# Performance work log

Measured on AMD Instinct MI355X. Metric: run time of the kernel, lower is better.

## Reference

```python
import jax, jax.numpy as jnp
import numpy as np

B, DIM_IN, DIM_OUT, K, A, P = 4, 128, 128, 13, 12, 1024


def _icosahedron_indices():
    """Rebuild the trace/inv index buffers of BasicS2Conv from icosahedron geometry.
    Returns kidx3, aidx3 of shape (K, A, A) = (13, 12, 12) such that the doubly-gathered
    weight is W_full[d,c,k,a,r] = W[d,c, kidx3[k,a,r], aidx3[k,a,r]]."""
    phi = (1.0 + 5.0 ** 0.5) / 2.0
    vs = []
    for s1 in (1.0, -1.0):
        for s2 in (1.0, -1.0):
            vs += [[0.0, s1, s2 * phi], [s1, s2 * phi, 0.0], [s2 * phi, 0.0, s1]]
    vs = np.asarray(vs, dtype=np.float64)
    vs /= np.linalg.norm(vs, axis=1, keepdims=True)
    dots = vs @ vs.T
    order = np.argsort(-dots, axis=1)
    v_adjs = order[:, 1:6]      # 5 adjacent vertices (dot = +1/sqrt5)
    v_level2s = order[:, 6:11]  # 5 second-ring vertices (dot = -1/sqrt5)
    v_opps = order[:, 11]       # antipodal vertex

    def frame(i):
        z = vs[i]
        a = vs[v_adjs[i, 0]]
        x = a - (a @ z) * z
        x /= np.linalg.norm(x)
        y = np.cross(z, x)
        return np.stack([x, y, z], axis=1)

    F0 = frame(0)
    Rs = np.stack([frame(i) @ F0.T for i in range(A)])  # 12 vertex-aligned rotations
    sim = np.einsum('rij,aj,bi->rab', Rs, vs, vs)       # <R_r v_a, v_b>
    trace_idx_rot = np.argmax(sim, axis=1)              # (12, 12) permutations

    inv_idxs = np.empty(K, dtype=np.int64)
    inv_idxs[0] = 0
    inv_idxs[v_adjs[0]] = 1
    inv_idxs[v_level2s[0]] = 2
    inv_idxs[v_opps[0]] = 3
    inv_idxs[12] = 4

    trace_idxv_rot = np.concatenate([trace_idx_rot, np.full((A, 1), 12, dtype=np.int64)], axis=1)  # (12, 13)
    kidx = inv_idxs[trace_idxv_rot].T  # (13, 12): kidx[k, r]
    aidx = trace_idx_rot.T             # (12, 12): aidx[a, r]
    kidx3 = np.broadcast_to(kidx[:, None, :], (K, A, A)).copy()
    aidx3 = np.broadcast_to(aidx[None, :, :], (K, A, A)).copy()
    return kidx3.astype(np.int32), aidx3.astype(np.int32)


def setup_inputs() -> dict:
    key = jax.random.key(0)
    kx, kw = jax.random.split(key)
    x = jax.random.normal(kx, (B, DIM_IN, K, P, A), dtype=jnp.float32)
    # xavier-normal-ish scale for W (dim_out, dim_in, 5, anchor)
    fan = DIM_IN * 5 * A + DIM_OUT * 5 * A
    std = (2.0 ** 0.5) * (2.0 / fan) ** 0.5
    W = jax.random.normal(kw, (DIM_OUT, DIM_IN, 5, A), dtype=jnp.float32) * std
    kidx3, aidx3 = _icosahedron_indices()
    return {"x": x, "W": W, "kidx": jnp.asarray(kidx3), "aidx": jnp.asarray(aidx3)}


def reference(x, W, kidx, aidx):
    # Double gather: W (d, c, 5, A) -> W_full (d, c, K, A, A_rot)
    # W_full[d, c, k, a, r] = W[d, c, kidx[k, a, r], aidx[k, a, r]]
    W_full = W[:, :, kidx, aidx]
    # contraction over kernel point k, input channel c, anchor a
    return jnp.einsum('dckar,bckpa->bdpr', W_full, x)
```

## Files before the change

### kernel.cpp

```cpp
#include <hip/hip_runtime.h>
#include <hip/hip_bf16.h>

typedef __bf16 bf16x8 __attribute__((ext_vector_type(8)));
typedef __bf16 bf16x4 __attribute__((ext_vector_type(4)));
typedef float f32x4 __attribute__((ext_vector_type(4)));
typedef float f32x3 __attribute__((ext_vector_type(3)));
typedef unsigned int u32x3 __attribute__((ext_vector_type(3)));
typedef unsigned short u16;
typedef unsigned int u32;

#define B_   4
#define C_   128
#define K_   13
#define A_   12
#define P_   1024
#define D_   128
#define R_   12
#define NB   1024

#define AS1 __attribute__((address_space(1)))
#define AS3 __attribute__((address_space(3)))

__device__ __forceinline__ u16 f2bf(float f) {
    u32 u = __builtin_bit_cast(u32, f);
    u32 r = (u + 0x7FFFu + ((u >> 16) & 1u)) >> 16;
    return (u16)r;
}
__device__ __forceinline__ float bf2f(u16 v) {
    u32 u = (u32)v << 16;
    return __builtin_bit_cast(float, u);
}
__device__ __forceinline__ u32 pack2(float lo, float hi) {
    return (u32)f2bf(lo) | ((u32)f2bf(hi) << 16);
}

__device__ __forceinline__ void barrier_() {
    asm volatile("" ::: "memory");
    __builtin_amdgcn_s_barrier();
    asm volatile("" ::: "memory");
}
__device__ __forceinline__ void lgkm0_() {
    asm volatile("s_waitcnt lgkmcnt(0)" ::: "memory");
    __builtin_amdgcn_sched_barrier(0);
}
#define VMW(n) asm volatile("s_waitcnt vmcnt(" #n ")" ::: "memory")

__global__ __launch_bounds__(512) void poolk_b(const float* __restrict__ xb_,
                                               const int* __restrict__ kidx3,
                                               u16* __restrict__ pool) {
    const int c  = blockIdx.x;
    const int pp = blockIdx.y;
    const int t  = threadIdx.x;
    const int ah = t & 1, aoff = ah * 6;

    u32 m1[12];
#pragma unroll
    for (int k = 0; k < 12; ++k) {
        u32 m = 0;
#pragma unroll
        for (int r = 0; r < 12; ++r)
            m |= (kidx3[k * 144 + r] == 1 ? 1u : 0u) << r;
        m1[k] = m;
    }

    const float* xb = xb_ + (size_t)c * (K_ * (size_t)P_ * A_);
    const size_t cslab   = (size_t)c * NB * 12;
    const size_t jstride = (size_t)C_ * NB * 12;

    int p = pp * 256 + (t >> 1);
    size_t obase = cslab + (size_t)p * 12 + aoff;
    float T[6] = {0.f, 0.f, 0.f, 0.f, 0.f, 0.f};
    float N[12][6];
#pragma unroll
    for (int r = 0; r < 12; ++r)
#pragma unroll
        for (int j = 0; j < 6; ++j) N[r][j] = 0.f;

#pragma unroll
    for (int k = 0; k < 13; ++k) {
        const float* s = xb + (size_t)k * (P_ * A_) + p * 12 + aoff;
        f32x3 v0 = *(const f32x3*)s;
        f32x3 v1 = *(const f32x3*)(s + 3);
        float v[6] = {v0.x, v0.y, v0.z, v1.x, v1.y, v1.z};
        u32x3 o;
        o.x = pack2(v[0], v[1]); o.y = pack2(v[2], v[3]); o.z = pack2(v[4], v[5]);
        *(u32x3*)(pool + (size_t)k * jstride + obase) = o;
        if (k < 12) {
#pragma unroll
            for (int j = 0; j < 6; ++j) T[j] += v[j];
            u32 m = m1[k];
#pragma unroll
            for (int r = 0; r < 12; ++r) {
                if (m & (1u << r)) {
#pragma unroll
                    for (int j = 0; j < 6; ++j) N[r][j] += v[j];
                }
            }
        }
    }
    {
        u32x3 o;
        o.x = pack2(T[0], T[1]); o.y = pack2(T[2], T[3]); o.z = pack2(T[4], T[5]);
        *(u32x3*)(pool + (size_t)13 * jstride + obase) = o;
    }
#pragma unroll
    for (int r = 0; r < 12; ++r) {
        u32x3 o;
        o.x = pack2(N[r][0], N[r][1]); o.y = pack2(N[r][2], N[r][3]); o.z = pack2(N[r][4], N[r][5]);
        *(u32x3*)(pool + (size_t)(14 + r) * jstride + obase) = o;
    }
}

__global__ __launch_bounds__(256) void abuild(const float* __restrict__ W,
                                              const int* __restrict__ aidx3,
                                              u16* __restrict__ Ab) {
    int gidx = blockIdx.x * 256 + threadIdx.x;
    int r   = gidx / (128 * 960);
    int rem = gidx - r * (128 * 960);
    int d   = rem / 960;
    int p8  = rem - d * 960;
    int phys = p8 * 8;
    int tile = phys / 96;
    int w96  = phys - tile * 96;
    int ks   = w96 >> 5;
    int chp  = (w96 >> 3) & 3;
    int ch   = chp ^ ((d >> 1) & 3);
    int qbase = tile * 96 + ks * 32 + ch * 8;
    u16 o[8];
#pragma unroll
    for (int e = 0; e < 8; ++e) {
        int q  = qbase + e;
        int g  = q / 1536;
        int qq = q - g * 1536;
        int c  = qq / 12;
        int a  = qq - c * 12;
        int aa = aidx3[a * 12 + r];
        const float* wb = W + ((size_t)(d * C_ + c) * 5) * 12 + aa;
        float val;
        if (g == 2)      val = wb[2 * 12];
        else if (g == 4) val = wb[4 * 12];
        else             val = wb[g * 12] - wb[2 * 12];
        o[e] = f2bf(val);
    }
    uint4 v;
    v.x = (u32)o[0] | ((u32)o[1] << 16);
    v.y = (u32)o[2] | ((u32)o[3] << 16);
    v.z = (u32)o[4] | ((u32)o[5] << 16);
    v.w = (u32)o[6] | ((u32)o[7] << 16);
    *(uint4*)(Ab + (((size_t)(r * 80 + tile) * 128 + d) * 96 + w96)) = v;
}

__global__ __launch_bounds__(512) void gemmSb(const u16* __restrict__ Ab,
                                              const u16* __restrict__ pool,
                                              const int* __restrict__ kidx3,
                                              u16* __restrict__ Ctb) {
    __shared__ __align__(16) u16 sA[2][128 * 96];
    __shared__ __align__(16) u16 sB[2][8 * 256 * 12];

    int bx = blockIdx.x;
    int r  = bx % 12;
    int nt = (bx / 12) & 3;
    int sp = bx / 48;
    int n0 = nt * 256;

    int k0r = 0, k3r = 0;
    for (int k = 0; k < 13; ++k) {
        int kv = kidx3[k * 144 + r];
        if (kv == 0) k0r = k;
        if (kv == 3) k3r = k;
    }
    int j = (sp == 0) ? k0r : (sp == 1) ? (14 + r) : (sp == 2) ? 13
          : (sp == 3) ? k3r : 12;

    int lane = threadIdx.x & 63;
    int w    = threadIdx.x >> 6;
    int wm   = w >> 2, wn = w & 3;
    int lq   = lane & 15;

    auto stageA = [&](int buf, int u) {
        const char* src = (const char*)(Ab + (size_t)(r * 80 + sp * 16 + u) * (128 * 96))
                        + w * 3072 + lane * 16;
#pragma unroll
        for (int i = 0; i < 3; ++i)
            __builtin_amdgcn_global_load_lds(
                (const AS1 void*)(src + i * 1024),
                (AS3 void*)&sA[buf][w * 1536 + i * 512],
                16, 0, 0);
    };
    auto stageB = [&](int buf, int u) {
        const char* src = (const char*)(pool + ((size_t)(j * C_ + u * 8 + w) * NB + n0) * 12)
                        + lane * 16;
#pragma unroll
        for (int i = 0; i < 6; ++i)
            __builtin_amdgcn_global_load_lds(
                (const AS1 void*)(src + i * 1024),
                (AS3 void*)&sB[buf][w * 3072 + i * 512],
                16, 0, 0);
    };
    auto ldA = [&](int buf, int m, int ks) -> bf16x8 {
        int ch = (lane >> 4) ^ ((m >> 1) & 3);
        return *(const bf16x8*)&sA[buf][m * 96 + ks * 32 + ch * 8];
    };
    auto ldB = [&](int buf, int n, int ks) -> bf16x8 {
        int q0 = ks * 32 + (lane >> 4) * 8;
        int c1 = q0 / 12, a1 = q0 - c1 * 12;
        int q2 = q0 + 4;
        int c2 = q2 / 12, a2 = q2 - c2 * 12;
        bf16x4 lo = *(const bf16x4*)&sB[buf][c1 * 3072 + n * 12 + a1];
        bf16x4 hi = *(const bf16x4*)&sB[buf][c2 * 3072 + n * 12 + a2];
        return __builtin_shufflevector(lo, hi, 0, 1, 2, 3, 4, 5, 6, 7);
    };

    f32x4 acc[4][4];
#pragma unroll
    for (int i = 0; i < 4; ++i)
#pragma unroll
        for (int jj = 0; jj < 4; ++jj) acc[i][jj] = (f32x4){0.f, 0.f, 0.f, 0.f};

    const int NTL = 16;
    stageA(0, 0);
    stageB(0, 0);

    for (int u = 0; u < NTL; ++u) {
        int cur = u & 1;
        if (u + 1 < NTL) {
            stageA(cur ^ 1, u + 1);
            stageB(cur ^ 1, u + 1);
            VMW(9);
        } else {
            VMW(0);
        }
        barrier_();
#pragma unroll
        for (int ks = 0; ks < 3; ++ks) {
            bf16x8 af[4], bf_[4];
#pragma unroll
            for (int mf = 0; mf < 4; ++mf)
                af[mf] = ldA(cur, wm * 64 + mf * 16 + lq, ks);
#pragma unroll
            for (int nf = 0; nf < 4; ++nf)
                bf_[nf] = ldB(cur, wn * 64 + nf * 16 + lq, ks);
            lgkm0_();
            __builtin_amdgcn_s_setprio(1);
#pragma unroll
            for (int mf = 0; mf < 4; ++mf)
#pragma unroll
                for (int nf = 0; nf < 4; ++nf)
                    acc[mf][nf] = __builtin_amdgcn_mfma_f32_16x16x32_bf16(
                        af[mf], bf_[nf], acc[mf][nf], 0, 0, 0);
            __builtin_amdgcn_s_setprio(0);
        }
        barrier_();
    }

    u16* Cs = Ctb + (size_t)sp * (1536 * (size_t)NB);
#pragma unroll
    for (int mf = 0; mf < 4; ++mf)
#pragma unroll
        for (int nf = 0; nf < 4; ++nf) {
            int col = n0 + wn * 64 + nf * 16 + lq;
#pragma unroll
            for (int v = 0; v < 4; ++v) {
                int drow = wm * 64 + mf * 16 + ((lane >> 4) << 2) + v;
                Cs[(size_t)(r * 128 + drow) * NB + col] = f2bf(acc[mf][nf][v]);
            }
        }
}

__global__ __launch_bounds__(256) void pass4c(const u16* __restrict__ Ct,
                                              float* __restrict__ out) {
    __shared__ float lds[12 * 256];
    int bid = blockIdx.x;
    int pch = bid & 3;
    int d   = (bid >> 2) & 127;
    int b   = bid >> 9;
    int p0  = pch * 256;
    int t   = threadIdx.x;
#pragma unroll
    for (int r = 0; r < 12; ++r) {
        float s = 0.f;
#pragma unroll
        for (int sp = 0; sp < 5; ++sp) {
            size_t idx = ((size_t)(b * 5 + sp) * 1536 + (r * 128 + d)) * NB + p0 + t;
            s += bf2f(Ct[idx]);
        }
        lds[r * 256 + t] = s;
    }
    __syncthreads();
    float* obase = out + ((size_t)((b * D_ + d) * P_ + p0)) * 12;
#pragma unroll
    for (int q = 0; q < 3; ++q) {
        int e0 = q * 1024 + t * 4;
        float4 v;
        { int e = e0 + 0; int p = e / 12; int r = e - p * 12; v.x = lds[r * 256 + p]; }
        { int e = e0 + 1; int p = e / 12; int r = e - p * 12; v.y = lds[r * 256 + p]; }
        { int e = e0 + 2; int p = e / 12; int r = e - p * 12; v.z = lds[r * 256 + p]; }
        { int e = e0 + 3; int p = e / 12; int r = e - p * 12; v.w = lds[r * 256 + p]; }
        *(float4*)(obase + e0) = v;
    }
}

__global__ __launch_bounds__(256) void naive_kernel(const float* __restrict__ x,
                                                    const float* __restrict__ W,
                                                    const int* __restrict__ kidx3,
                                                    const int* __restrict__ aidx3,
                                                    float* __restrict__ out) {
    long long t = (long long)blockIdx.x * 256 + threadIdx.x;
    if (t >= (long long)B_ * D_ * P_ * R_) return;
    int r = (int)(t % 12);
    int p = (int)((t / 12) % P_);
    int d = (int)((t / (12 * P_)) % D_);
    int b = (int)(t / (12 * (long long)P_ * D_));
    int kk[K_];
    int aa[A_];
#pragma unroll
    for (int k = 0; k < K_; ++k) kk[k] = kidx3[(k * 12 + 0) * 12 + r];
#pragma unroll
    for (int a = 0; a < A_; ++a) aa[a] = aidx3[(0 * 12 + a) * 12 + r];
    float sum = 0.f;
    for (int c = 0; c < C_; ++c) {
        const float* wrow = W + (size_t)(d * C_ + c) * 60;
        const float* xrow = x + ((size_t)(b * C_ + c) * K_) * (P_ * A_) + (size_t)p * A_;
        for (int k = 0; k < K_; ++k) {
            const float* wk = wrow + kk[k] * 12;
            const float* xk = xrow + (size_t)k * (P_ * A_);
#pragma unroll
            for (int a = 0; a < A_; ++a) sum += wk[aa[a]] * xk[a];
        }
    }
    out[t] = sum;
}

extern "C" void kernel_launch(void* const* d_in, const int* in_sizes, int n_in,
                              void* d_out, int out_size, void* d_ws, size_t ws_size,
                              hipStream_t stream) {
    const float* x     = (const float*)d_in[0];
    const float* W     = (const float*)d_in[1];
    const int*   kidx3 = (const int*)d_in[2];
    const int*   aidx3 = (const int*)d_in[3];
    float*       out   = (float*)d_out;

    const size_t POOLB = (size_t)26 * C_ * NB * 12 * 2;
    const size_t AB    = (size_t)12 * 80 * 128 * 96 * 2;
    const size_t CT5   = (size_t)B_ * 5 * 1536 * NB * 2;

    if (ws_size >= POOLB + AB + CT5) {
        u16* pool = (u16*)d_ws;
        u16* Abuf = (u16*)((char*)d_ws + POOLB);
        u16* Ct   = (u16*)((char*)d_ws + POOLB + AB);
        abuild<<<5760, 256, 0, stream>>>(W, aidx3, Abuf);
        for (int b = 0; b < 4; ++b) {
            const float* xb = x + (size_t)b * C_ * K_ * P_ * A_;
            u16* Ctb = Ct + (size_t)b * 5 * 1536 * NB;
            poolk_b<<<dim3(128, 4), 512, 0, stream>>>(xb, kidx3, pool);
            gemmSb<<<240, 512, 0, stream>>>(Abuf, pool, kidx3, Ctb);
        }
        pass4c<<<2048, 256, 0, stream>>>(Ct, out);
    } else {
        naive_kernel<<<(B_ * D_ * P_ * R_) / 256, 256, 0, stream>>>(x, W, kidx3, aidx3, out);
    }
}
```

Measured before the change: 392.6 us.

## Batch all four inputs into one pooling and one GEMM launch with split-K by four

```diff
diff --git a/kernel.cpp b/kernel.cpp
--- a/kernel.cpp
+++ b/kernel.cpp
@@ -16,7 +16,9 @@
 #define P_   1024
 #define D_   128
 #define R_   12
-#define NB   1024
+#define MT   1536
+#define NT   4096
+#define KP   7680
 
 #define AS1 __attribute__((address_space(1)))
 #define AS3 __attribute__((address_space(3)))
@@ -45,12 +47,12 @@
 }
 #define VMW(n) asm volatile("s_waitcnt vmcnt(" #n ")" ::: "memory")
 
-__global__ __launch_bounds__(512) void poolk_b(const float* __restrict__ xb_,
-                                               const int* __restrict__ kidx3,
-                                               u16* __restrict__ pool) {
-    const int c  = blockIdx.x;
-    const int pp = blockIdx.y;
-    const int t  = threadIdx.x;
+__global__ __launch_bounds__(512) void poolk(const float* __restrict__ x,
+                                             const int* __restrict__ kidx3,
+                                             u16* __restrict__ pool) {
+    const int c = blockIdx.x;
+    const int b = blockIdx.y;
+    const int t = threadIdx.x;
     const int ah = t & 1, aoff = ah * 6;
 
     u32 m1[12];
@@ -63,51 +65,54 @@
         m1[k] = m;
     }
 
-    const float* xb = xb_ + (size_t)c * (K_ * (size_t)P_ * A_);
-    const size_t cslab   = (size_t)c * NB * 12;
-    const size_t jstride = (size_t)C_ * NB * 12;
-
-    int p = pp * 256 + (t >> 1);
-    size_t obase = cslab + (size_t)p * 12 + aoff;
-    float T[6] = {0.f, 0.f, 0.f, 0.f, 0.f, 0.f};
-    float N[12][6];
-#pragma unroll
-    for (int r = 0; r < 12; ++r)
-#pragma unroll
-        for (int j = 0; j < 6; ++j) N[r][j] = 0.f;
-
-#pragma unroll
-    for (int k = 0; k < 13; ++k) {
-        const float* s = xb + (size_t)k * (P_ * A_) + p * 12 + aoff;
-        f32x3 v0 = *(const f32x3*)s;
-        f32x3 v1 = *(const f32x3*)(s + 3);
-        float v[6] = {v0.x, v0.y, v0.z, v1.x, v1.y, v1.z};
-        u32x3 o;
-        o.x = pack2(v[0], v[1]); o.y = pack2(v[2], v[3]); o.z = pack2(v[4], v[5]);
-        *(u32x3*)(pool + (size_t)k * jstride + obase) = o;
-        if (k < 12) {
-#pragma unroll
-            for (int j = 0; j < 6; ++j) T[j] += v[j];
-            u32 m = m1[k];
-#pragma unroll
-            for (int r = 0; r < 12; ++r) {
-                if (m & (1u << r)) {
-#pragma unroll
-                    for (int j = 0; j < 6; ++j) N[r][j] += v[j];
+    const float* xb = x + (size_t)(b * C_ + c) * (K_ * (size_t)P_ * A_);
+    const size_t cslab = ((size_t)c * 4096) * 12;
+    const size_t jstride = (size_t)C_ * 4096 * 12;
+
+    for (int pp = 0; pp < 4; ++pp) {
+        int p = pp * 256 + (t >> 1);
+        int n = b * P_ + p;
+        size_t obase = cslab + (size_t)n * 12 + aoff;
+        float T[6] = {0.f, 0.f, 0.f, 0.f, 0.f, 0.f};
+        float N[12][6];
+#pragma unroll
+        for (int r = 0; r < 12; ++r)
+#pragma unroll
+            for (int j = 0; j < 6; ++j) N[r][j] = 0.f;
+
+#pragma unroll
+        for (int k = 0; k < 13; ++k) {
+            const float* s = xb + (size_t)k * (P_ * A_) + p * 12 + aoff;
+            f32x3 v0 = *(const f32x3*)s;
+            f32x3 v1 = *(const f32x3*)(s + 3);
+            float v[6] = {v0.x, v0.y, v0.z, v1.x, v1.y, v1.z};
+            u32x3 o;
+            o.x = pack2(v[0], v[1]); o.y = pack2(v[2], v[3]); o.z = pack2(v[4], v[5]);
+            *(u32x3*)(pool + (size_t)k * jstride + obase) = o;
+            if (k < 12) {
+#pragma unroll
+                for (int j = 0; j < 6; ++j) T[j] += v[j];
+                u32 m = m1[k];
+#pragma unroll
+                for (int r = 0; r < 12; ++r) {
+                    if (m & (1u << r)) {
+#pragma unroll
+                        for (int j = 0; j < 6; ++j) N[r][j] += v[j];
+                    }
                 }
             }
         }
-    }
-    {
-        u32x3 o;
-        o.x = pack2(T[0], T[1]); o.y = pack2(T[2], T[3]); o.z = pack2(T[4], T[5]);
-        *(u32x3*)(pool + (size_t)13 * jstride + obase) = o;
-    }
-#pragma unroll
-    for (int r = 0; r < 12; ++r) {
-        u32x3 o;
-        o.x = pack2(N[r][0], N[r][1]); o.y = pack2(N[r][2], N[r][3]); o.z = pack2(N[r][4], N[r][5]);
-        *(u32x3*)(pool + (size_t)(14 + r) * jstride + obase) = o;
+        {
+            u32x3 o;
+            o.x = pack2(T[0], T[1]); o.y = pack2(T[2], T[3]); o.z = pack2(T[4], T[5]);
+            *(u32x3*)(pool + (size_t)13 * jstride + obase) = o;
+        }
+#pragma unroll
+        for (int r = 0; r < 12; ++r) {
+            u32x3 o;
+            o.x = pack2(N[r][0], N[r][1]); o.y = pack2(N[r][2], N[r][3]); o.z = pack2(N[r][4], N[r][5]);
+            *(u32x3*)(pool + (size_t)(14 + r) * jstride + obase) = o;
+        }
     }
 }
 
@@ -150,17 +155,17 @@
     *(uint4*)(Ab + (((size_t)(r * 80 + tile) * 128 + d) * 96 + w96)) = v;
 }
 
-__global__ __launch_bounds__(512) void gemmSb(const u16* __restrict__ Ab,
-                                              const u16* __restrict__ pool,
-                                              const int* __restrict__ kidx3,
-                                              u16* __restrict__ Ctb) {
+__global__ __launch_bounds__(512) void gemmS(const u16* __restrict__ Ab,
+                                             const u16* __restrict__ pool,
+                                             const int* __restrict__ kidx3,
+                                             u16* __restrict__ C) {
     __shared__ __align__(16) u16 sA[2][128 * 96];
     __shared__ __align__(16) u16 sB[2][8 * 256 * 12];
 
     int bx = blockIdx.x;
-    int r  = bx % 12;
-    int nt = (bx / 12) & 3;
-    int sp = bx / 48;
+    int nt = bx & 15;
+    int r  = (bx >> 4) % 12;
+    int sp = bx / 192;
     int n0 = nt * 256;
 
     int k0r = 0, k3r = 0;
@@ -169,16 +174,14 @@
         if (kv == 0) k0r = k;
         if (kv == 3) k3r = k;
     }
-    int j = (sp == 0) ? k0r : (sp == 1) ? (14 + r) : (sp == 2) ? 13
-          : (sp == 3) ? k3r : 12;
 
     int lane = threadIdx.x & 63;
     int w    = threadIdx.x >> 6;
     int wm   = w >> 2, wn = w & 3;
     int lq   = lane & 15;
 
-    auto stageA = [&](int buf, int u) {
-        const char* src = (const char*)(Ab + (size_t)(r * 80 + sp * 16 + u) * (128 * 96))
+    auto stageA = [&](int buf, int tile) {
+        const char* src = (const char*)(Ab + (size_t)(r * 80 + tile) * (128 * 96))
                         + w * 3072 + lane * 16;
 #pragma unroll
         for (int i = 0; i < 3; ++i)
@@ -187,8 +190,12 @@
                 (AS3 void*)&sA[buf][w * 1536 + i * 512],
                 16, 0, 0);
     };
-    auto stageB = [&](int buf, int u) {
-        const char* src = (const char*)(pool + ((size_t)(j * C_ + u * 8 + w) * NB + n0) * 12)
+    auto stageB = [&](int buf, int tile) {
+        int gt = tile >> 4;
+        int c  = ((tile & 15) << 3) + w;
+        int j  = (gt == 0) ? k0r : (gt == 1) ? (14 + r) : (gt == 2) ? 13
+               : (gt == 3) ? k3r : 12;
+        const char* src = (const char*)(pool + ((size_t)(j * C_ + c) * 4096 + n0) * 12)
                         + lane * 16;
 #pragma unroll
         for (int i = 0; i < 6; ++i)
@@ -215,17 +222,19 @@
 #pragma unroll
     for (int i = 0; i < 4; ++i)
 #pragma unroll
-        for (int jj = 0; jj < 4; ++jj) acc[i][jj] = (f32x4){0.f, 0.f, 0.f, 0.f};
-
-    const int NTL = 16;
-    stageA(0, 0);
-    stageB(0, 0);
-
-    for (int u = 0; u < NTL; ++u) {
+        for (int j = 0; j < 4; ++j) acc[i][j] = (f32x4){0.f, 0.f, 0.f, 0.f};
+
+    const int NTL2 = 20;
+    int t0 = sp * NTL2;
+
+    stageA(0, t0);
+    stageB(0, t0);
+
+    for (int u = 0; u < NTL2; ++u) {
         int cur = u & 1;
-        if (u + 1 < NTL) {
-            stageA(cur ^ 1, u + 1);
-            stageB(cur ^ 1, u + 1);
+        if (u + 1 < NTL2) {
+            stageA(cur ^ 1, t0 + u + 1);
+            stageB(cur ^ 1, t0 + u + 1);
             VMW(9);
         } else {
             VMW(0);
@@ -253,7 +262,7 @@
         barrier_();
     }
 
-    u16* Cs = Ctb + (size_t)sp * (1536 * (size_t)NB);
+    u16* Cs = C + (size_t)sp * ((size_t)MT * NT);
 #pragma unroll
     for (int mf = 0; mf < 4; ++mf)
 #pragma unroll
@@ -262,12 +271,13 @@
 #pragma unroll
             for (int v = 0; v < 4; ++v) {
                 int drow = wm * 64 + mf * 16 + ((lane >> 4) << 2) + v;
-                Cs[(size_t)(r * 128 + drow) * NB + col] = f2bf(acc[mf][nf][v]);
+                Cs[(size_t)(r * 128 + drow) * NT + col] = f2bf(acc[mf][nf][v]);
             }
         }
 }
 
-__global__ __launch_bounds__(256) void pass4c(const u16* __restrict__ Ct,
+template <int SPLIT>
+__global__ __launch_bounds__(256) void pass4b(const u16* __restrict__ Ct,
                                               float* __restrict__ out) {
     __shared__ float lds[12 * 256];
     int bid = blockIdx.x;
@@ -278,12 +288,11 @@
     int t   = threadIdx.x;
 #pragma unroll
     for (int r = 0; r < 12; ++r) {
+        size_t off = (size_t)(r * D_ + d) * NT + b * P_ + p0 + t;
         float s = 0.f;
 #pragma unroll
-        for (int sp = 0; sp < 5; ++sp) {
-            size_t idx = ((size_t)(b * 5 + sp) * 1536 + (r * 128 + d)) * NB + p0 + t;
-            s += bf2f(Ct[idx]);
-        }
+        for (int sp = 0; sp < SPLIT; ++sp)
+            s += bf2f(Ct[(size_t)sp * MT * NT + off]);
         lds[r * 256 + t] = s;
     }
     __syncthreads();
@@ -340,22 +349,18 @@
     const int*   aidx3 = (const int*)d_in[3];
     float*       out   = (float*)d_out;
 
-    const size_t POOLB = (size_t)26 * C_ * NB * 12 * 2;
-    const size_t AB    = (size_t)12 * 80 * 128 * 96 * 2;
-    const size_t CT5   = (size_t)B_ * 5 * 1536 * NB * 2;
-
-    if (ws_size >= POOLB + AB + CT5) {
+    const size_t POOL = (size_t)26 * C_ * 4096 * 12 * 2;
+    const size_t AB   = (size_t)12 * 80 * 128 * 96 * 2;
+    const size_t CTH  = (size_t)MT * NT * 2;
+
+    if (ws_size >= POOL + AB + 4 * CTH) {
         u16* pool = (u16*)d_ws;
-        u16* Abuf = (u16*)((char*)d_ws + POOLB);
-        u16* Ct   = (u16*)((char*)d_ws + POOLB + AB);
+        u16* Abuf = (u16*)((char*)d_ws + POOL);
+        u16* Ct   = (u16*)((char*)d_ws + POOL + AB);
+        poolk<<<dim3(128, 4), 512, 0, stream>>>(x, kidx3, pool);
         abuild<<<5760, 256, 0, stream>>>(W, aidx3, Abuf);
-        for (int b = 0; b < 4; ++b) {
-            const float* xb = x + (size_t)b * C_ * K_ * P_ * A_;
-            u16* Ctb = Ct + (size_t)b * 5 * 1536 * NB;
-            poolk_b<<<dim3(128, 4), 512, 0, stream>>>(xb, kidx3, pool);
-            gemmSb<<<240, 512, 0, stream>>>(Abuf, pool, kidx3, Ctb);
-        }
-        pass4c<<<2048, 256, 0, stream>>>(Ct, out);
+        gemmS<<<768, 512, 0, stream>>>(Abuf, pool, kidx3, Ct);
+        pass4b<4><<<2048, 256, 0, stream>>>(Ct, out);
     } else {
         naive_kernel<<<(B_ * D_ * P_ * R_) / 256, 256, 0, stream>>>(x, W, kidx3, aidx3, out);
     }
```

After: 364.2 us. 1.08x faster.
